# Performance work log

Measured on AMD Instinct MI355X. Metric: run time of the kernel, lower is better.

Reference implementation:

```python
import jax, jax.numpy as jnp
import numpy as np

E = 16      # num_experts
H = 1024    # hidden_dim
I = 2048    # intermediate_dim
K = 2       # top_k routing
T = 2048    # tokens


def setup_inputs() -> dict:
    key = jax.random.key(0)
    k0, k1, k2, k3, k4 = jax.random.split(key, 5)
    std = 0.02  # nn.init.normal_(std=0.02) in _create_new_expert
    return {
        "x": jax.random.normal(k0, (T, H), dtype=jnp.float32),
        "w_router": jax.random.normal(k1, (H, E), dtype=jnp.float32) * std,
        "w_gate": jax.random.normal(k2, (E, H, I), dtype=jnp.float32) * std,
        "w_up": jax.random.normal(k3, (E, H, I), dtype=jnp.float32) * std,
        "w_down": jax.random.normal(k4, (E, I, H), dtype=jnp.float32) * std,
    }


def reference(x, w_router, w_gate, w_up, w_down):
    # --- router: softmax gating, top-k selection, renormalized weights ---
    logits = x @ w_router                                   # [T, E]
    probs = jax.nn.softmax(logits, axis=-1)                 # [T, E]
    vals, idx = jax.lax.top_k(probs, K)                     # [T, K]
    vals = vals / jnp.sum(vals, axis=-1, keepdims=True)     # renormalize over top-k
    # sparse combine weights: zero outside selected experts  [T, E]
    combine = jnp.sum(jax.nn.one_hot(idx, E, dtype=x.dtype) * vals[..., None], axis=1)
    # --- per-expert SwiGLU FFN (dense-over-experts, masked combine) ---
    gate = jnp.einsum('th,ehi->tei', x, w_gate)             # [T, E, I]
    up = jnp.einsum('th,ehi->tei', x, w_up)                 # [T, E, I]
    hidden = jax.nn.silu(gate) * up * combine[:, :, None]   # fuse combine weight
    y = jnp.einsum('tei,eih->th', hidden, w_down)           # [T, H]
    return y
```

## Files before the change

kernel.cpp:

```cpp
#include <hip/hip_runtime.h>
#include <hip/hip_bf16.h>
#include <math.h>


#define T_TOK 2048
#define H_DIM 1024
#define I_DIM 2048
#define E_NUM 16
#define N_ASSIGN 4096
#define BM 128
#define TILE_MAX 48

typedef __attribute__((ext_vector_type(8))) short short8;
typedef __attribute__((ext_vector_type(4))) float floatx4;

#define WS_OFF_COUNTS   0
#define WS_OFF_OFFSETS  64
#define WS_OFF_TOPKIDX  256
#define WS_OFF_TOPKW    (WS_OFF_TOPKIDX + 16384)
#define WS_OFF_ROWTOK   (WS_OFF_TOPKW  + 16384)
#define WS_OFF_ROWW     (WS_OFF_ROWTOK + 16384)
#define WS_OFF_TILEE    (WS_OFF_ROWW   + 16384)
#define WS_OFF_TILEM    (WS_OFF_TILEE  + 256)
#define WS_OFF_TILEC    (WS_OFF_TILEM  + 256)
#define WS_OFF_XG       (128 * 1024)
#define WS_OFF_H1       (WS_OFF_XG + 8u * 1024 * 1024)

__device__ __forceinline__ ushort f2bf(float f) {
    union { float f; unsigned int u; } v; v.f = f;
    unsigned int r = (v.u + 0x7fffu + ((v.u >> 16) & 1u)) >> 16;
    return (ushort)r;
}

__global__ __launch_bounds__(64)
void router_kernel(const float* __restrict__ x,
                   const float* __restrict__ wr,
                   int* __restrict__ counts,
                   int* __restrict__ topk_idx,
                   float* __restrict__ topk_w) {
    const int t = blockIdx.x;
    const int lane = threadIdx.x;
    const float* xt = x + (size_t)t * H_DIM;

    float acc[E_NUM];
#pragma unroll
    for (int e = 0; e < E_NUM; e++) acc[e] = 0.f;

    for (int h = lane; h < H_DIM; h += 64) {
        const float xv = xt[h];
        const float* wrow = wr + h * E_NUM;
#pragma unroll
        for (int e = 0; e < E_NUM; e++) acc[e] += xv * wrow[e];
    }
#pragma unroll
    for (int off = 32; off > 0; off >>= 1) {
#pragma unroll
        for (int e = 0; e < E_NUM; e++)
            acc[e] += __shfl_down(acc[e], off);
    }
    if (lane == 0) {
        int e0 = 0; float l0 = acc[0];
        for (int e = 1; e < E_NUM; e++)
            if (acc[e] > l0) { l0 = acc[e]; e0 = e; }
        int e1 = (e0 == 0) ? 1 : 0;
        float l1 = acc[e1];
        for (int e = 0; e < E_NUM; e++)
            if (e != e0 && acc[e] > l1) { l1 = acc[e]; e1 = e; }
        const float w0 = 1.f / (1.f + __expf(l1 - l0));
        const float w1 = 1.f - w0;
        topk_idx[t * 2 + 0] = e0;
        topk_idx[t * 2 + 1] = e1;
        topk_w[t * 2 + 0] = w0;
        topk_w[t * 2 + 1] = w1;
        atomicAdd(&counts[e0], 1);
        atomicAdd(&counts[e1], 1);
    }
}

__global__ __launch_bounds__(256)
void scatter_kernel(const int* __restrict__ counts,
                    int* __restrict__ offsets,
                    const int* __restrict__ topk_idx,
                    const float* __restrict__ topk_w,
                    int* __restrict__ row_token,
                    float* __restrict__ row_w,
                    int* __restrict__ tile_e,
                    int* __restrict__ tile_m,
                    int* __restrict__ tile_c) {
    __shared__ int base[E_NUM];
    __shared__ int fill[E_NUM];
    const int tid = threadIdx.x;
    if (tid == 0) {
        int run = 0, tc = 0;
        for (int e = 0; e < E_NUM; e++) {
            offsets[e] = run;
            base[e] = run;
            const int cnt = counts[e];
            run += cnt;
            for (int m = 0; m * BM < cnt; m++) {
                tile_e[tc] = e;
                tile_m[tc] = m;
                tc++;
            }
        }
        offsets[E_NUM] = run;
        *tile_c = tc;
    }
    if (tid < E_NUM) fill[tid] = 0;
    __syncthreads();
    for (int a = tid; a < N_ASSIGN; a += blockDim.x) {
        const int e = topk_idx[a];
        const int pos = atomicAdd(&fill[e], 1);
        const int dst = base[e] + pos;
        row_token[dst] = a >> 1;
        row_w[dst] = topk_w[a];
    }
}

__global__ __launch_bounds__(256)
void gather_x_kernel(const float* __restrict__ x,
                     const int* __restrict__ row_token,
                     ushort* __restrict__ Xg) {
    const int r = blockIdx.x;
    const int t = row_token[r];
    const int c = threadIdx.x;
    floatx4 v = ((const floatx4*)(x + (size_t)t * H_DIM))[c];
    ushort4 o;
    o.x = f2bf(v[0]); o.y = f2bf(v[1]); o.z = f2bf(v[2]); o.w = f2bf(v[3]);
    ((ushort4*)(Xg + (size_t)r * H_DIM))[c] = o;
}

__global__ __launch_bounds__(256)
void gemm_gu_kernel(const ushort* __restrict__ Xg,
                    const float* __restrict__ wg,
                    const float* __restrict__ wu,
                    const int* __restrict__ offsets,
                    const float* __restrict__ row_w,
                    const int* __restrict__ tile_e,
                    const int* __restrict__ tile_m,
                    const int* __restrict__ tile_c,
                    ushort* __restrict__ h1) {
    if ((int)blockIdx.y >= *tile_c) return;
    const int e     = tile_e[blockIdx.y];
    const int mtile = tile_m[blockIdx.y];
    const int ntile = blockIdx.x;
    const int beg = offsets[e];
    const int n   = offsets[e + 1] - beg;

    __shared__ ushort As[BM * 32];
    __shared__ ushort Bgs[64 * 40];
    __shared__ ushort Bus[64 * 40];
    __shared__ float  wts[BM];

    const int tid  = threadIdx.x;
    const int lane = tid & 63;
    const int w    = tid >> 6;
    const int ml   = lane & 15;
    const int q    = lane >> 4;

    if (tid < BM) {
        const int rl = mtile * BM + tid;
        wts[tid] = (rl < n) ? row_w[beg + rl] : 0.f;
    }

    floatx4 accg[2][4], accu[2][4];
#pragma unroll
    for (int i = 0; i < 2; i++)
#pragma unroll
        for (int j = 0; j < 4; j++) {
            accg[i][j] = (floatx4){0.f, 0.f, 0.f, 0.f};
            accu[i][j] = (floatx4){0.f, 0.f, 0.f, 0.f};
        }

    const ushort* Ap[2];
#pragma unroll
    for (int j = 0; j < 2; j++) {
        int row = beg + mtile * BM + 32 * w + 16 * j + (lane >> 2);
        row = row < 4095 ? row : 4095;
        Ap[j] = Xg + (size_t)row * H_DIM + (lane & 3) * 8;
    }

    const int kh = tid & 15;
    const int n4 = tid >> 4;
    const float* Bgp = wg + (size_t)e * H_DIM * I_DIM + ntile * 64 + n4 * 4;
    const float* Bup = wu + (size_t)e * H_DIM * I_DIM + ntile * 64 + n4 * 4;

    for (int k0 = 0; k0 < H_DIM; k0 += 32) {
#pragma unroll
        for (int j = 0; j < 2; j++)
            __builtin_amdgcn_global_load_lds(
                (const __attribute__((address_space(1))) unsigned int*)(Ap[j] + k0),
                (__attribute__((address_space(3))) unsigned int*)(As + (32 * w + 16 * j) * 32),
                16, 0, 0);

        const size_t boff = (size_t)(k0 + 2 * kh) * I_DIM;
        floatx4 g0 = *(const floatx4*)(Bgp + boff);
        floatx4 g1 = *(const floatx4*)(Bgp + boff + I_DIM);
        floatx4 u0 = *(const floatx4*)(Bup + boff);
        floatx4 u1 = *(const floatx4*)(Bup + boff + I_DIM);
#pragma unroll
        for (int j2 = 0; j2 < 4; j2++) {
            unsigned int pg = (unsigned int)f2bf(g0[j2]) |
                              ((unsigned int)f2bf(g1[j2]) << 16);
            unsigned int pu = (unsigned int)f2bf(u0[j2]) |
                              ((unsigned int)f2bf(u1[j2]) << 16);
            *(unsigned int*)&Bgs[(n4 * 4 + j2) * 40 + 2 * kh] = pg;
            *(unsigned int*)&Bus[(n4 * 4 + j2) * 40 + 2 * kh] = pu;
        }
        __syncthreads();

        short8 af[2], bg[4], bu[4];
#pragma unroll
        for (int mt = 0; mt < 2; mt++)
            af[mt] = *(const short8*)&As[(32 * w + mt * 16 + ml) * 32 + q * 8];
#pragma unroll
        for (int nt = 0; nt < 4; nt++) {
            bg[nt] = *(const short8*)&Bgs[(nt * 16 + ml) * 40 + q * 8];
            bu[nt] = *(const short8*)&Bus[(nt * 16 + ml) * 40 + q * 8];
        }
#pragma unroll
        for (int mt = 0; mt < 2; mt++)
#pragma unroll
            for (int nt = 0; nt < 4; nt++) {
                accg[mt][nt] = __builtin_amdgcn_mfma_f32_16x16x32_bf16(
                    af[mt], bg[nt], accg[mt][nt], 0, 0, 0);
                accu[mt][nt] = __builtin_amdgcn_mfma_f32_16x16x32_bf16(
                    af[mt], bu[nt], accu[mt][nt], 0, 0, 0);
            }
        __syncthreads();
    }

#pragma unroll
    for (int mt = 0; mt < 2; mt++)
#pragma unroll
        for (int r = 0; r < 4; r++) {
            const int rloc = 32 * w + mt * 16 + q * 4 + r;
            const int rl = mtile * BM + rloc;
            if (rl < n) {
                const float cw = wts[rloc];
#pragma unroll
                for (int nt = 0; nt < 4; nt++) {
                    const float g = accg[mt][nt][r];
                    const float s = g / (1.f + __expf(-g));
                    h1[(size_t)(beg + rl) * I_DIM + ntile * 64 + nt * 16 + ml] =
                        f2bf(s * accu[mt][nt][r] * cw);
                }
            }
        }
}

__global__ __launch_bounds__(256)
void gemm_down_kernel(const ushort* __restrict__ h1,
                      const float* __restrict__ wd,
                      const int* __restrict__ offsets,
                      const int* __restrict__ row_token,
                      const int* __restrict__ tile_e,
                      const int* __restrict__ tile_m,
                      const int* __restrict__ tile_c,
                      float* __restrict__ y) {
    if ((int)blockIdx.y >= *tile_c) return;
    const int e     = tile_e[blockIdx.y];
    const int mtile = tile_m[blockIdx.y];
    const int ntile = blockIdx.x;
    const int kbase = blockIdx.z * 1024;
    const int beg = offsets[e];
    const int n   = offsets[e + 1] - beg;

    __shared__ ushort As[BM * 32];
    __shared__ ushort Bs[64 * 40];
    __shared__ int    toks[BM];

    const int tid  = threadIdx.x;
    const int lane = tid & 63;
    const int w    = tid >> 6;
    const int ml   = lane & 15;
    const int q    = lane >> 4;

    if (tid < BM) {
        const int rl = mtile * BM + tid;
        toks[tid] = (rl < n) ? row_token[beg + rl] : 0;
    }

    floatx4 acc[2][4];
#pragma unroll
    for (int i = 0; i < 2; i++)
#pragma unroll
        for (int j = 0; j < 4; j++) acc[i][j] = (floatx4){0.f, 0.f, 0.f, 0.f};

    const ushort* Ap[2];
#pragma unroll
    for (int j = 0; j < 2; j++) {
        int row = beg + mtile * BM + 32 * w + 16 * j + (lane >> 2);
        row = row < 4095 ? row : 4095;
        Ap[j] = h1 + (size_t)row * I_DIM + kbase + (lane & 3) * 8;
    }

    const int kh = tid & 15;
    const int n4 = tid >> 4;
    const float* Bp = wd + (size_t)e * I_DIM * H_DIM +
                      (size_t)kbase * H_DIM + ntile * 64 + n4 * 4;

    for (int k0 = 0; k0 < 1024; k0 += 32) {
#pragma unroll
        for (int j = 0; j < 2; j++)
            __builtin_amdgcn_global_load_lds(
                (const __attribute__((address_space(1))) unsigned int*)(Ap[j] + k0),
                (__attribute__((address_space(3))) unsigned int*)(As + (32 * w + 16 * j) * 32),
                16, 0, 0);

        const size_t boff = (size_t)(k0 + 2 * kh) * H_DIM;
        floatx4 b0 = *(const floatx4*)(Bp + boff);
        floatx4 b1 = *(const floatx4*)(Bp + boff + H_DIM);
#pragma unroll
        for (int j2 = 0; j2 < 4; j2++) {
            unsigned int p = (unsigned int)f2bf(b0[j2]) |
                             ((unsigned int)f2bf(b1[j2]) << 16);
            *(unsigned int*)&Bs[(n4 * 4 + j2) * 40 + 2 * kh] = p;
        }
        __syncthreads();

        short8 af[2], bfr[4];
#pragma unroll
        for (int mt = 0; mt < 2; mt++)
            af[mt] = *(const short8*)&As[(32 * w + mt * 16 + ml) * 32 + q * 8];
#pragma unroll
        for (int nt = 0; nt < 4; nt++)
            bfr[nt] = *(const short8*)&Bs[(nt * 16 + ml) * 40 + q * 8];
#pragma unroll
        for (int mt = 0; mt < 2; mt++)
#pragma unroll
            for (int nt = 0; nt < 4; nt++)
                acc[mt][nt] = __builtin_amdgcn_mfma_f32_16x16x32_bf16(
                    af[mt], bfr[nt], acc[mt][nt], 0, 0, 0);
        __syncthreads();
    }

#pragma unroll
    for (int mt = 0; mt < 2; mt++)
#pragma unroll
        for (int r = 0; r < 4; r++) {
            const int rloc = 32 * w + mt * 16 + q * 4 + r;
            const int rl = mtile * BM + rloc;
            if (rl < n) {
                const int t = toks[rloc];
#pragma unroll
                for (int nt = 0; nt < 4; nt++)
                    atomicAdd(&y[(size_t)t * H_DIM + ntile * 64 + nt * 16 + ml],
                              acc[mt][nt][r]);
            }
        }
}

extern "C" void kernel_launch(void* const* d_in, const int* in_sizes, int n_in,
                              void* d_out, int out_size, void* d_ws, size_t ws_size,
                              hipStream_t stream) {
    const float* x  = (const float*)d_in[0];
    const float* wr = (const float*)d_in[1];
    const float* wg = (const float*)d_in[2];
    const float* wu = (const float*)d_in[3];
    const float* wd = (const float*)d_in[4];
    float* y = (float*)d_out;

    char* ws = (char*)d_ws;
    int*    counts    = (int*)(ws + WS_OFF_COUNTS);
    int*    offsets   = (int*)(ws + WS_OFF_OFFSETS);
    int*    topk_idx  = (int*)(ws + WS_OFF_TOPKIDX);
    float*  topk_w    = (float*)(ws + WS_OFF_TOPKW);
    int*    row_token = (int*)(ws + WS_OFF_ROWTOK);
    float*  row_w     = (float*)(ws + WS_OFF_ROWW);
    int*    tile_e    = (int*)(ws + WS_OFF_TILEE);
    int*    tile_m    = (int*)(ws + WS_OFF_TILEM);
    int*    tile_c    = (int*)(ws + WS_OFF_TILEC);
    ushort* Xg        = (ushort*)(ws + WS_OFF_XG);
    ushort* h1        = (ushort*)(ws + WS_OFF_H1);

    hipMemsetAsync(counts, 0, 64, stream);
    hipMemsetAsync(y, 0, (size_t)T_TOK * H_DIM * sizeof(float), stream);

    router_kernel<<<T_TOK, 64, 0, stream>>>(x, wr, counts, topk_idx, topk_w);
    scatter_kernel<<<1, 256, 0, stream>>>(counts, offsets, topk_idx, topk_w,
                                          row_token, row_w, tile_e, tile_m, tile_c);
    gather_x_kernel<<<N_ASSIGN, 256, 0, stream>>>(x, row_token, Xg);
    gemm_gu_kernel<<<dim3(I_DIM / 64, TILE_MAX), 256, 0, stream>>>(
        Xg, wg, wu, offsets, row_w, tile_e, tile_m, tile_c, h1);
    gemm_down_kernel<<<dim3(H_DIM / 64, TILE_MAX, 2), 256, 0, stream>>>(
        h1, wd, offsets, row_token, tile_e, tile_m, tile_c, y);
}
```

Before: 565.3 us.

## Double-buffer LDS tiles with software-pipelined prefetch and swizzled A layout in expert GEMMs

Both expert GEMM kernels now use double-buffered shared-memory tiles, prefetching the next two K-steps of activations (via global_load_lds) and weights into registers while MFMAs run on the current buffer. Explicit vmcnt waits replace the full syncthreads pair, along with a single barrier per step and s_setprio around the MFMA block. The A-tile columns are XOR-swizzled to cut LDS bank conflicts. The aim is to hide global-load latency behind compute. The cost is doubled LDS use, which may lower occupancy, and hand-counted waitcnts that are fragile; the wrapped prefetch addresses at the end of K cause redundant loads.

```diff
diff --git a/kernel.cpp b/kernel.cpp
--- a/kernel.cpp
+++ b/kernel.cpp
@@ -31,6 +31,15 @@
     unsigned int r = (v.u + 0x7fffu + ((v.u >> 16) & 1u)) >> 16;
     return (ushort)r;
 }
+
+#define FENCE_LGKM0() asm volatile("s_waitcnt lgkmcnt(0)" ::: "memory")
+#define WAIT_VM(N)    asm volatile("s_waitcnt vmcnt(" #N ")" ::: "memory")
+#define BARRIER_()                                    \
+    do {                                              \
+        FENCE_LGKM0();                                \
+        __builtin_amdgcn_s_barrier();                 \
+        asm volatile("" ::: "memory");                \
+    } while (0)
 
 __global__ __launch_bounds__(64)
 void router_kernel(const float* __restrict__ x,
@@ -147,9 +156,9 @@
     const int beg = offsets[e];
     const int n   = offsets[e + 1] - beg;
 
-    __shared__ ushort As[BM * 32];
-    __shared__ ushort Bgs[64 * 40];
-    __shared__ ushort Bus[64 * 40];
+    __shared__ ushort As[2][BM * 32];
+    __shared__ ushort Bgs[2][64 * 40];
+    __shared__ ushort Bus[2][64 * 40];
     __shared__ float  wts[BM];
 
     const int tid  = threadIdx.x;
@@ -157,6 +166,8 @@
     const int w    = tid >> 6;
     const int ml   = lane & 15;
     const int q    = lane >> 4;
+    const int rq   = (ml >> 1) & 3;
+    const int srcq = (lane & 3) ^ ((lane >> 3) & 3);
 
     if (tid < BM) {
         const int rl = mtile * BM + tid;
@@ -177,7 +188,7 @@
     for (int j = 0; j < 2; j++) {
         int row = beg + mtile * BM + 32 * w + 16 * j + (lane >> 2);
         row = row < 4095 ? row : 4095;
-        Ap[j] = Xg + (size_t)row * H_DIM + (lane & 3) * 8;
+        Ap[j] = Xg + (size_t)row * H_DIM + srcq * 8;
     }
 
     const int kh = tid & 15;
@@ -185,50 +196,91 @@
     const float* Bgp = wg + (size_t)e * H_DIM * I_DIM + ntile * 64 + n4 * 4;
     const float* Bup = wu + (size_t)e * H_DIM * I_DIM + ntile * 64 + n4 * 4;
 
-    for (int k0 = 0; k0 < H_DIM; k0 += 32) {
-#pragma unroll
-        for (int j = 0; j < 2; j++)
-            __builtin_amdgcn_global_load_lds(
-                (const __attribute__((address_space(1))) unsigned int*)(Ap[j] + k0),
-                (__attribute__((address_space(3))) unsigned int*)(As + (32 * w + 16 * j) * 32),
-                16, 0, 0);
-
-        const size_t boff = (size_t)(k0 + 2 * kh) * I_DIM;
-        floatx4 g0 = *(const floatx4*)(Bgp + boff);
-        floatx4 g1 = *(const floatx4*)(Bgp + boff + I_DIM);
-        floatx4 u0 = *(const floatx4*)(Bup + boff);
-        floatx4 u1 = *(const floatx4*)(Bup + boff + I_DIM);
-#pragma unroll
-        for (int j2 = 0; j2 < 4; j2++) {
-            unsigned int pg = (unsigned int)f2bf(g0[j2]) |
-                              ((unsigned int)f2bf(g1[j2]) << 16);
-            unsigned int pu = (unsigned int)f2bf(u0[j2]) |
-                              ((unsigned int)f2bf(u1[j2]) << 16);
-            *(unsigned int*)&Bgs[(n4 * 4 + j2) * 40 + 2 * kh] = pg;
-            *(unsigned int*)&Bus[(n4 * 4 + j2) * 40 + 2 * kh] = pu;
-        }
-        __syncthreads();
-
-        short8 af[2], bg[4], bu[4];
-#pragma unroll
-        for (int mt = 0; mt < 2; mt++)
-            af[mt] = *(const short8*)&As[(32 * w + mt * 16 + ml) * 32 + q * 8];
-#pragma unroll
-        for (int nt = 0; nt < 4; nt++) {
-            bg[nt] = *(const short8*)&Bgs[(nt * 16 + ml) * 40 + q * 8];
-            bu[nt] = *(const short8*)&Bus[(nt * 16 + ml) * 40 + q * 8];
-        }
-#pragma unroll
-        for (int mt = 0; mt < 2; mt++)
-#pragma unroll
-            for (int nt = 0; nt < 4; nt++) {
-                accg[mt][nt] = __builtin_amdgcn_mfma_f32_16x16x32_bf16(
-                    af[mt], bg[nt], accg[mt][nt], 0, 0, 0);
-                accu[mt][nt] = __builtin_amdgcn_mfma_f32_16x16x32_bf16(
-                    af[mt], bu[nt], accu[mt][nt], 0, 0, 0);
-            }
-        __syncthreads();
-    }
+    floatx4 g0p, g1p, u0p, u1p, g0q, g1q, u0q, u1q;
+
+#define GU_ISSUE_A(k0v, buf)                                                   \
+    {                                                                          \
+        __builtin_amdgcn_global_load_lds(                                      \
+            (const __attribute__((address_space(1))) unsigned int*)(Ap[0] + (k0v)), \
+            (__attribute__((address_space(3))) unsigned int*)(&As[buf][(32 * w) * 32]), \
+            16, 0, 0);                                                         \
+        __builtin_amdgcn_global_load_lds(                                      \
+            (const __attribute__((address_space(1))) unsigned int*)(Ap[1] + (k0v)), \
+            (__attribute__((address_space(3))) unsigned int*)(&As[buf][(32 * w + 16) * 32]), \
+            16, 0, 0);                                                         \
+    }
+
+#define GU_ISSUE_B(k0v, G0, G1, U0, U1)                                        \
+    {                                                                          \
+        const size_t boff = (size_t)((k0v) + 2 * kh) * I_DIM;                  \
+        G0 = *(const floatx4*)(Bgp + boff);                                    \
+        G1 = *(const floatx4*)(Bgp + boff + I_DIM);                            \
+        U0 = *(const floatx4*)(Bup + boff);                                    \
+        U1 = *(const floatx4*)(Bup + boff + I_DIM);                            \
+    }
+
+#define GU_CVT_B(buf, G0, G1, U0, U1)                                          \
+    {                                                                          \
+        _Pragma("unroll")                                                      \
+        for (int j2 = 0; j2 < 4; j2++) {                                       \
+            unsigned int pg = (unsigned int)f2bf(G0[j2]) |                     \
+                              ((unsigned int)f2bf(G1[j2]) << 16);              \
+            unsigned int pu = (unsigned int)f2bf(U0[j2]) |                     \
+                              ((unsigned int)f2bf(U1[j2]) << 16);              \
+            *(unsigned int*)&Bgs[buf][(n4 * 4 + j2) * 40 + 2 * kh] = pg;       \
+            *(unsigned int*)&Bus[buf][(n4 * 4 + j2) * 40 + 2 * kh] = pu;       \
+        }                                                                      \
+    }
+
+    GU_ISSUE_B(0, g0p, g1p, u0p, u1p);
+    GU_ISSUE_A(0, 0);
+    GU_ISSUE_B(32, g0q, g1q, u0q, u1q);
+    GU_ISSUE_A(32, 1);
+    WAIT_VM(6);
+    GU_CVT_B(0, g0p, g1p, u0p, u1p);
+    BARRIER_();
+
+#define GU_STEP(cur, kpre, CG0, CG1, CU0, CU1, PG0, PG1, PU0, PU1)             \
+    {                                                                          \
+        short8 af[2], bgf[4], buf4[4];                                         \
+        _Pragma("unroll")                                                      \
+        for (int mt = 0; mt < 2; mt++)                                         \
+            af[mt] = *(const short8*)&As[cur][(32 * w + mt * 16 + ml) * 32 +   \
+                                              ((q ^ rq) * 8)];                 \
+        FENCE_LGKM0();             \
+        GU_ISSUE_B(kpre, PG0, PG1, PU0, PU1);                                  \
+        GU_ISSUE_A(kpre, cur);                                                 \
+        _Pragma("unroll")                                                      \
+        for (int nt = 0; nt < 4; nt++) {                                       \
+            bgf[nt]  = *(const short8*)&Bgs[cur][(nt * 16 + ml) * 40 + q * 8]; \
+            buf4[nt] = *(const short8*)&Bus[cur][(nt * 16 + ml) * 40 + q * 8]; \
+        }                                                                      \
+        __builtin_amdgcn_s_setprio(1);                                         \
+        _Pragma("unroll")                                                      \
+        for (int mt = 0; mt < 2; mt++)                                         \
+            _Pragma("unroll")                                                  \
+            for (int nt = 0; nt < 4; nt++) {                                   \
+                accg[mt][nt] = __builtin_amdgcn_mfma_f32_16x16x32_bf16(        \
+                    af[mt], bgf[nt], accg[mt][nt], 0, 0, 0);                   \
+                accu[mt][nt] = __builtin_amdgcn_mfma_f32_16x16x32_bf16(        \
+                    af[mt], buf4[nt], accu[mt][nt], 0, 0, 0);                  \
+            }                                                                  \
+        __builtin_amdgcn_s_setprio(0);                                         \
+        WAIT_VM(6);                                                            \
+        GU_CVT_B(cur ^ 1, CG0, CG1, CU0, CU1);                                 \
+        BARRIER_();                                                            \
+    }
+
+    for (int k0 = 0; k0 < H_DIM; k0 += 64) {
+        const int kpe = (k0 + 64) & (H_DIM - 1);
+        const int kpo = (k0 + 96) & (H_DIM - 1);
+        GU_STEP(0, kpe, g0q, g1q, u0q, u1q, g0p, g1p, u0p, u1p);
+        GU_STEP(1, kpo, g0p, g1p, u0p, u1p, g0q, g1q, u0q, u1q);
+    }
+#undef GU_STEP
+#undef GU_CVT_B
+#undef GU_ISSUE_B
+#undef GU_ISSUE_A
 
 #pragma unroll
     for (int mt = 0; mt < 2; mt++)
@@ -266,8 +318,8 @@
     const int beg = offsets[e];
     const int n   = offsets[e + 1] - beg;
 
-    __shared__ ushort As[BM * 32];
-    __shared__ ushort Bs[64 * 40];
+    __shared__ ushort As[2][BM * 32];
+    __shared__ ushort Bs[2][64 * 40];
     __shared__ int    toks[BM];
 
     const int tid  = threadIdx.x;
@@ -275,6 +327,8 @@
     const int w    = tid >> 6;
     const int ml   = lane & 15;
     const int q    = lane >> 4;
+    const int rq   = (ml >> 1) & 3;
+    const int srcq = (lane & 3) ^ ((lane >> 3) & 3);
 
     if (tid < BM) {
         const int rl = mtile * BM + tid;
@@ -292,7 +346,7 @@
     for (int j = 0; j < 2; j++) {
         int row = beg + mtile * BM + 32 * w + 16 * j + (lane >> 2);
         row = row < 4095 ? row : 4095;
-        Ap[j] = h1 + (size_t)row * I_DIM + kbase + (lane & 3) * 8;
+        Ap[j] = h1 + (size_t)row * I_DIM + kbase + srcq * 8;
     }
 
     const int kh = tid & 15;
@@ -300,40 +354,81 @@
     const float* Bp = wd + (size_t)e * I_DIM * H_DIM +
                       (size_t)kbase * H_DIM + ntile * 64 + n4 * 4;
 
-    for (int k0 = 0; k0 < 1024; k0 += 32) {
-#pragma unroll
-        for (int j = 0; j < 2; j++)
-            __builtin_amdgcn_global_load_lds(
-                (const __attribute__((address_space(1))) unsigned int*)(Ap[j] + k0),
-                (__attribute__((address_space(3))) unsigned int*)(As + (32 * w + 16 * j) * 32),
-                16, 0, 0);
-
-        const size_t boff = (size_t)(k0 + 2 * kh) * H_DIM;
-        floatx4 b0 = *(const floatx4*)(Bp + boff);
-        floatx4 b1 = *(const floatx4*)(Bp + boff + H_DIM);
-#pragma unroll
-        for (int j2 = 0; j2 < 4; j2++) {
-            unsigned int p = (unsigned int)f2bf(b0[j2]) |
-                             ((unsigned int)f2bf(b1[j2]) << 16);
-            *(unsigned int*)&Bs[(n4 * 4 + j2) * 40 + 2 * kh] = p;
-        }
-        __syncthreads();
-
-        short8 af[2], bfr[4];
-#pragma unroll
-        for (int mt = 0; mt < 2; mt++)
-            af[mt] = *(const short8*)&As[(32 * w + mt * 16 + ml) * 32 + q * 8];
-#pragma unroll
-        for (int nt = 0; nt < 4; nt++)
-            bfr[nt] = *(const short8*)&Bs[(nt * 16 + ml) * 40 + q * 8];
-#pragma unroll
-        for (int mt = 0; mt < 2; mt++)
-#pragma unroll
-            for (int nt = 0; nt < 4; nt++)
-                acc[mt][nt] = __builtin_amdgcn_mfma_f32_16x16x32_bf16(
-                    af[mt], bfr[nt], acc[mt][nt], 0, 0, 0);
-        __syncthreads();
-    }
+    floatx4 b0p, b1p, b0q, b1q;
+
+#define D_ISSUE_A(k0v, buf)                                                    \
+    {                                                                          \
+        __builtin_amdgcn_global_load_lds(                                      \
+            (const __attribute__((address_space(1))) unsigned int*)(Ap[0] + (k0v)), \
+            (__attribute__((address_space(3))) unsigned int*)(&As[buf][(32 * w) * 32]), \
+            16, 0, 0);                                                         \
+        __builtin_amdgcn_global_load_lds(                                      \
+            (const __attribute__((address_space(1))) unsigned int*)(Ap[1] + (k0v)), \
+            (__attribute__((address_space(3))) unsigned int*)(&As[buf][(32 * w + 16) * 32]), \
+            16, 0, 0);                                                         \
+    }
+
+#define D_ISSUE_B(k0v, B0, B1)                                                 \
+    {                                                                          \
+        const size_t boff = (size_t)((k0v) + 2 * kh) * H_DIM;                  \
+        B0 = *(const floatx4*)(Bp + boff);                                     \
+        B1 = *(const floatx4*)(Bp + boff + H_DIM);                             \
+    }
+
+#define D_CVT_B(buf, B0, B1)                                                   \
+    {                                                                          \
+        _Pragma("unroll")                                                      \
+        for (int j2 = 0; j2 < 4; j2++) {                                       \
+            unsigned int p = (unsigned int)f2bf(B0[j2]) |                      \
+                             ((unsigned int)f2bf(B1[j2]) << 16);               \
+            *(unsigned int*)&Bs[buf][(n4 * 4 + j2) * 40 + 2 * kh] = p;         \
+        }                                                                      \
+    }
+
+    D_ISSUE_B(0, b0p, b1p);
+    D_ISSUE_A(0, 0);
+    D_ISSUE_B(32, b0q, b1q);
+    D_ISSUE_A(32, 1);
+    WAIT_VM(4);
+    D_CVT_B(0, b0p, b1p);
+    BARRIER_();
+
+#define D_STEP(cur, kpre, CB0, CB1, PB0, PB1)                                  \
+    {                                                                          \
+        short8 af[2], bfr[4];                                                  \
+        _Pragma("unroll")                                                      \
+        for (int mt = 0; mt < 2; mt++)                                         \
+            af[mt] = *(const short8*)&As[cur][(32 * w + mt * 16 + ml) * 32 +   \
+                                              ((q ^ rq) * 8)];                 \
+        FENCE_LGKM0();                                                         \
+        D_ISSUE_B(kpre, PB0, PB1);                                             \
+        D_ISSUE_A(kpre, cur);                                                  \
+        _Pragma("unroll")                                                      \
+        for (int nt = 0; nt < 4; nt++)                                         \
+            bfr[nt] = *(const short8*)&Bs[cur][(nt * 16 + ml) * 40 + q * 8];   \
+        __builtin_amdgcn_s_setprio(1);                                         \
+        _Pragma("unroll")                                                      \
+        for (int mt = 0; mt < 2; mt++)                                         \
+            _Pragma("unroll")                                                  \
+            for (int nt = 0; nt < 4; nt++)                                     \
+                acc[mt][nt] = __builtin_amdgcn_mfma_f32_16x16x32_bf16(         \
+                    af[mt], bfr[nt], acc[mt][nt], 0, 0, 0);                    \
+        __builtin_amdgcn_s_setprio(0);                                         \
+        WAIT_VM(4);                                                            \
+        D_CVT_B(cur ^ 1, CB0, CB1);                                            \
+        BARRIER_();                                                            \
+    }
+
+    for (int k0 = 0; k0 < 1024; k0 += 64) {
+        const int kpe = (k0 + 64) & 1023;
+        const int kpo = (k0 + 96) & 1023;
+        D_STEP(0, kpe, b0q, b1q, b0p, b1p);
+        D_STEP(1, kpo, b0p, b1p, b0q, b1q);
+    }
+#undef D_STEP
+#undef D_CVT_B
+#undef D_ISSUE_B
+#undef D_ISSUE_A
 
 #pragma unroll
     for (int mt = 0; mt < 2; mt++)
```

New measurement: 579.7 us. 1.03x slower.
